# Kernel optimization log

Measured on AMD Instinct MI355X. Metric: run time of the kernel, lower is better.

The kernel has to match this reference:

```python
import jax, jax.numpy as jnp
import numpy as np

B, S, V, H, L, NH, DH, F, T = 256, 64, 21128, 768, 12, 12, 64, 3072, 11


def _layernorm(x, g, b):
    m = x.mean(-1, keepdims=True)
    v = ((x - m) ** 2).mean(-1, keepdims=True)
    return (x - m) / jnp.sqrt(v + 1e-12) * g + b


def setup_inputs():
    key = jax.random.key(0)
    ks = iter(jax.random.split(key, 24))
    std = 0.02
    w = lambda shape: jax.random.normal(next(ks), shape, jnp.float32) * std
    return {
        "input_ids": jax.random.randint(next(ks), (B, S), 0, V),
        "attention_mask": jnp.ones((B, S), jnp.int32),
        "label": jax.random.randint(next(ks), (B, S), 0, T),
        "word_emb": w((V, H)),
        "pos_emb": w((S, H)),
        "tok_emb": w((2, H)),
        "emb_ln_g": jnp.ones((H,), jnp.float32),
        "emb_ln_b": jnp.zeros((H,), jnp.float32),
        "Wqkv": w((L, H, 3 * H)),
        "bqkv": jnp.zeros((L, 3 * H), jnp.float32),
        "Wo": w((L, H, H)),
        "bo": jnp.zeros((L, H), jnp.float32),
        "ln1_g": jnp.ones((L, H), jnp.float32),
        "ln1_b": jnp.zeros((L, H), jnp.float32),
        "W1": w((L, H, F)),
        "b1": jnp.zeros((L, F), jnp.float32),
        "W2": w((L, F, H)),
        "b2": jnp.zeros((L, H), jnp.float32),
        "ln2_g": jnp.ones((L, H), jnp.float32),
        "ln2_b": jnp.zeros((L, H), jnp.float32),
        "fc_w": w((H, T)),
        "fc_b": jnp.zeros((T,), jnp.float32),
        "crf_start": w((T,)),
        "crf_end": w((T,)),
        "crf_trans": w((T, T)),
    }


def _encode(ids, mask, word_emb, pos_emb, tok_emb, eg, eb, layer_params):
    x = word_emb[ids] + pos_emb[None] + tok_emb[0][None, None]  # [B,S,H]
    x = _layernorm(x, eg, eb)
    bias = (1.0 - mask.astype(x.dtype))[:, None, None, :] * -1e9  # [B,1,1,S]

    def layer(x, p):
        Wqkv, bqkv, Wo, bo, g1, b1n, W1, b1, W2, b2, g2, b2n = p
        q, k, v = jnp.split(x @ Wqkv + bqkv, 3, axis=-1)
        sh = lambda t: t.reshape(B, S, NH, DH).transpose(0, 2, 1, 3)
        att = jax.nn.softmax(
            jnp.einsum("bhqd,bhkd->bhqk", sh(q), sh(k)) / jnp.sqrt(jnp.float32(DH)) + bias, -1
        )
        o = jnp.einsum("bhqk,bhkd->bhqd", att, sh(v)).transpose(0, 2, 1, 3).reshape(B, S, H)
        x = _layernorm(x + o @ Wo + bo, g1, b1n)
        h = jax.nn.gelu(x @ W1 + b1)
        x = _layernorm(x + h @ W2 + b2, g2, b2n)
        return x, None

    x, _ = jax.lax.scan(layer, x, layer_params)
    return x


def _crf_llh(em, tags, maskf, start, end, trans):
    # torchcrf log-likelihood, batch_first. em:[B,S,T] tags:[B,S] maskf:[B,S]
    bidx = jnp.arange(B)
    score = start[tags[:, 0]] + em[bidx, 0, tags[:, 0]]

    def num_step(s, xs):
        e_t, tp, tc, m = xs
        return s + (trans[tp, tc] + e_t[bidx, tc]) * m, None

    score, _ = jax.lax.scan(
        num_step, score,
        (em[:, 1:].transpose(1, 0, 2), tags[:, :-1].T, tags[:, 1:].T, maskf[:, 1:].T),
    )
    last_idx = maskf.sum(-1).astype(jnp.int32) - 1
    score = score + end[tags[bidx, last_idx]]

    alpha = start[None] + em[:, 0]  # [B,T]

    def den_step(a, xs):
        e_t, m = xs
        nxt = jax.scipy.special.logsumexp(a[:, :, None] + trans[None] + e_t[:, None, :], axis=1)
        return jnp.where(m[:, None] > 0, nxt, a), None

    alpha, _ = jax.lax.scan(den_step, alpha, (em[:, 1:].transpose(1, 0, 2), maskf[:, 1:].T))
    denom = jax.scipy.special.logsumexp(alpha + end[None], axis=1)
    return score - denom


def _viterbi(em, maskf, start, end, trans):
    bidx = jnp.arange(B)

    def step(s, xs):
        e_t, m = xs
        cand = s[:, :, None] + trans[None]  # [B,T_prev,T_cur]
        best_prev = jnp.argmax(cand, axis=1)  # [B,T]
        ns = jnp.max(cand, axis=1) + e_t
        return jnp.where(m[:, None] > 0, ns, s), best_prev

    score, hist = jax.lax.scan(
        step, start[None] + em[:, 0], (em[:, 1:].transpose(1, 0, 2), maskf[:, 1:].T)
    )  # hist: [S-1,B,T]
    last = jnp.argmax(score + end[None], axis=1)  # [B]

    def back(t, xs):
        h, m = xs
        nt = jnp.where(m > 0, h[bidx, t], t)
        return nt, nt

    _, prev_tags = jax.lax.scan(back, last, (hist, maskf[:, 1:].T), reverse=True)
    return jnp.concatenate([prev_tags.transpose(1, 0), last[:, None]], axis=1)  # [B,S]


def reference(input_ids, attention_mask, label, word_emb, pos_emb, tok_emb, emb_ln_g, emb_ln_b,
              Wqkv, bqkv, Wo, bo, ln1_g, ln1_b, W1, b1, W2, b2, ln2_g, ln2_b,
              fc_w, fc_b, crf_start, crf_end, crf_trans):
    lp = (Wqkv, bqkv, Wo, bo, ln1_g, ln1_b, W1, b1, W2, b2, ln2_g, ln2_b)
    x = _encode(input_ids, attention_mask, word_emb, pos_emb, tok_emb, emb_ln_g, emb_ln_b, lp)
    logits = x @ fc_w + fc_b  # [B,S,T]
    maskf = attention_mask.astype(jnp.float32)
    loss = -jnp.mean(_crf_llh(logits, label, maskf, crf_start, crf_end, crf_trans))
    pred = _viterbi(logits, maskf, crf_start, crf_end, crf_trans)
    return pred, loss
```

## Files before the change

kernel.cpp:

```cpp
#include <hip/hip_runtime.h>
#include <hip/hip_bf16.h>
#include <math.h>

namespace {

constexpr int B = 256, S = 64, H = 768, L = 12, NH = 12, F = 3072, T = 11;
constexpr int BS = B * S;
constexpr int RC = 8192;
constexpr int NCH = BS / RC;

typedef __attribute__((ext_vector_type(8))) short short8;
typedef __attribute__((ext_vector_type(4))) float f32x4;

__device__ __forceinline__ float gelu_tanh(float v) {
  float u = 0.7978845608028654f * (v + 0.044715f * v * v * v);
  u = fminf(fmaxf(u, -10.f), 10.f);
  float t = __expf(2.f * u);
  return 0.5f * v * (1.0f + (t - 1.f) / (t + 1.f));
}

__device__ __forceinline__ ushort f2bf(float v) {
  union { float f; unsigned u; } c; c.f = v;
  unsigned r = (c.u + 0x7fffu + ((c.u >> 16) & 1u)) >> 16;
  return (ushort)r;
}
__device__ __forceinline__ float bf2f(ushort u) {
  union { unsigned u; float f; } c; c.u = ((unsigned)u) << 16;
  return c.f;
}
__device__ __forceinline__ uint packhl(float v) {
  ushort hi = f2bf(v);
  ushort lo = f2bf(v - bf2f(hi));
  return (uint)hi | ((uint)lo << 16);
}
__device__ __forceinline__ float unpackhl(uint u) {
  union { unsigned u; float f; } a, b;
  a.u = u << 16;
  b.u = u & 0xffff0000u;
  return a.f + b.f;
}

__device__ __forceinline__ uint prm(uint a, uint b, uint s) {
#if __has_builtin(__builtin_amdgcn_perm)
  return __builtin_amdgcn_perm(a, b, s);
#else
  uint r = 0;
  for (int i = 0; i < 4; ++i) {
    uint sel = (s >> (8 * i)) & 0xff;
    uint byte = sel < 4 ? (b >> (8 * sel)) & 0xff : (a >> (8 * (sel - 4))) & 0xff;
    r |= byte << (8 * i);
  }
  return r;
#endif
}

union S8U { uint u[4]; short8 s; };

__device__ __forceinline__ void unpack_frag(uint4 v0, uint4 v1, short8& hi, short8& lo) {
  S8U h, l;
  h.u[0] = prm(v0.y, v0.x, 0x05040100u);
  l.u[0] = prm(v0.y, v0.x, 0x07060302u);
  h.u[1] = prm(v0.w, v0.z, 0x05040100u);
  l.u[1] = prm(v0.w, v0.z, 0x07060302u);
  h.u[2] = prm(v1.y, v1.x, 0x05040100u);
  l.u[2] = prm(v1.y, v1.x, 0x07060302u);
  h.u[3] = prm(v1.w, v1.z, 0x05040100u);
  l.u[3] = prm(v1.w, v1.z, 0x07060302u);
  hi = h.s;
  lo = l.s;
}

#define GLOAD_LDS16(gptr, ldsptr)                                                        \
  __builtin_amdgcn_global_load_lds((const __attribute__((address_space(1))) void*)(gptr), \
                                   (__attribute__((address_space(3))) void*)(ldsptr), 16, 0, 0)

template <int MODE>
__global__ __launch_bounds__(256, 2) void gemm_mfma(const uint* __restrict__ A,
                                                    const ushort* __restrict__ Bw,
                                                    const float* __restrict__ bias,
                                                    float* __restrict__ outF,
                                                    uint* __restrict__ outU,
                                                    int lda, int ldb2, int ldc,
                                                    int ldcF, int zStrideF, int ktiles) {
  __shared__ uint sA[2][128 * 32];
  __shared__ ushort sB[2][128 * 64];
  const int tid = threadIdx.x;
  const int w = tid >> 6;
  const int lane = tid & 63;
  const int wm = w >> 1;
  const int wn = w & 1;

  const int gx = gridDim.x, gy = gridDim.y;
  const int flat = ((int)blockIdx.z * gy + blockIdx.y) * gx + blockIdx.x;
  const int q8 = (gx * gy * (int)gridDim.z) >> 3;
  const int swz = (flat & 7) * q8 + (flat >> 3);
  const int bx = swz % gx;
  const int by = (swz / gx) % gy;
  const int bz = swz / (gx * gy);
  const int bm = by * 128;
  const int bn = bx * 128;
  const int kA0 = bz * ktiles * 32;
  const int kB0 = bz * ktiles * 64;

  const int srow = lane >> 3;
  const int sblk = (lane & 7) ^ srow;
  const uint* Ab = A + (size_t)(bm + w * 32 + srow) * lda + kA0 + sblk * 4;
  const ushort* Bb = Bw + (size_t)(bn + w * 32 + srow) * ldb2 + kB0 + sblk * 8;

#define STAGE(buf, tk)                                                            \
  do {                                                                            \
    _Pragma("unroll") for (int i_ = 0; i_ < 4; ++i_) {                            \
      GLOAD_LDS16(Ab + (size_t)(tk) * 32 + (size_t)(i_ * 8) * lda,                \
                  &sA[buf][(w * 32 + i_ * 8) * 32]);                              \
      GLOAD_LDS16(Bb + (size_t)(tk) * 64 + (size_t)(i_ * 8) * ldb2,               \
                  &sB[buf][(w * 32 + i_ * 8) * 64]);                              \
    }                                                                             \
  } while (0)

  const int fr = lane & 15;
  const int s7 = fr & 7;
  const int jb = lane >> 4;
  const int p0 = ((jb << 1) ^ s7) << 2;
  const int p1 = (((jb << 1) ^ s7) ^ 1) << 2;
  const int bhOff = (jb ^ s7) << 3;
  const int blOff = ((4 + jb) ^ s7) << 3;

  f32x4 acc[4][4] = {};
  const int NT = ktiles;

  STAGE(0, 0);
  asm volatile("s_waitcnt vmcnt(0)" ::: "memory");
  __builtin_amdgcn_s_barrier();

  for (int t = 0; t < NT; ++t) {
    const int cur = t & 1;
    if (t + 1 < NT) STAGE(cur ^ 1, t + 1);

    short8 ah[4], al[4];
#pragma unroll
    for (int mi = 0; mi < 4; ++mi) {
      const uint* baseA = &sA[cur][(wm * 64 + mi * 16 + fr) * 32];
      uint4 v0 = *(const uint4*)(baseA + p0);
      uint4 v1 = *(const uint4*)(baseA + p1);
      unpack_frag(v0, v1, ah[mi], al[mi]);
    }
#pragma unroll
    for (int ni = 0; ni < 4; ++ni) {
      const ushort* baseB = &sB[cur][(wn * 64 + ni * 16 + fr) * 64];
      short8 bh = *(const short8*)(baseB + bhOff);
      short8 bl = *(const short8*)(baseB + blOff);
      __builtin_amdgcn_s_setprio(1);
#pragma unroll
      for (int mi = 0; mi < 4; ++mi) {
        acc[mi][ni] = __builtin_amdgcn_mfma_f32_16x16x32_bf16(ah[mi], bh, acc[mi][ni], 0, 0, 0);
        acc[mi][ni] = __builtin_amdgcn_mfma_f32_16x16x32_bf16(ah[mi], bl, acc[mi][ni], 0, 0, 0);
        acc[mi][ni] = __builtin_amdgcn_mfma_f32_16x16x32_bf16(al[mi], bh, acc[mi][ni], 0, 0, 0);
      }
      __builtin_amdgcn_s_setprio(0);
      if (ni == 3) asm volatile("s_waitcnt vmcnt(0)" ::: "memory");
      __builtin_amdgcn_s_barrier();
    }
  }
#undef STAGE

  const int erow = jb << 2;
#pragma unroll
  for (int ni = 0; ni < 4; ++ni) {
    const int col = bn + wn * 64 + ni * 16 + fr;
    const float bv = (MODE == 3) ? 0.f : bias[col];
#pragma unroll
    for (int mi = 0; mi < 4; ++mi) {
#pragma unroll
      for (int e = 0; e < 4; ++e) {
        const int row = bm + wm * 64 + mi * 16 + erow + e;
        float v = acc[mi][ni][e] + bv;
        if (MODE == 1) {
          outU[(size_t)row * ldc + col] = packhl(gelu_tanh(v));
        } else if (MODE == 2) {
          outU[(size_t)row * ldc + col] = packhl(v);
        } else {
          outF[(size_t)bz * zStrideF + (size_t)row * ldcF + col] = v;
        }
      }
    }
  }
}

__global__ __launch_bounds__(256) void convert_w_t(const float* __restrict__ W,
                                                   ushort* __restrict__ WI, int K, int N) {
  __shared__ float tile[32][33];
  const int kb = blockIdx.y * 32, nb = blockIdx.x * 32;
  const int tr = threadIdx.x >> 5;
  const int tc = threadIdx.x & 31;
#pragma unroll
  for (int p = 0; p < 4; ++p) {
    int r = tr + p * 8;
    tile[r][tc] = W[(size_t)(kb + r) * N + nb + tc];
  }
  __syncthreads();
  const int kblk = kb >> 5;
#pragma unroll
  for (int p = 0; p < 4; ++p) {
    int n = tr + p * 8;
    float v = tile[tc][n];
    ushort hi = f2bf(v);
    ushort lo = f2bf(v - bf2f(hi));
    size_t o = (size_t)(nb + n) * (2 * K) + (size_t)kblk * 64 + tc;
    WI[o] = hi;
    WI[o + 32] = lo;
  }
}

__global__ __launch_bounds__(256) void attn_kernel(uint* __restrict__ qkv,
                                                   const int* __restrict__ mask) {
  __shared__ float smem[64 * 64 + 64 * 66 + 64 * 64];
  float (*Qs)[64] = (float (*)[64])smem;
  float (*KsT)[66] = (float (*)[66])(smem + 64 * 64);
  float (*Vs)[64] = (float (*)[64])(smem + 64 * 64 + 64 * 66);
  float (*Ps)[65] = (float (*)[65])smem;

  const int bl = blockIdx.x / NH;
  const int hh = blockIdx.x % NH;
  const int tid = threadIdx.x;
  const int lane = tid & 63;
  const int w = tid >> 6;

  for (int i = 0; i < 16; ++i) {
    int idx = tid + i * 256;
    int r = idx >> 6, d = idx & 63;
    size_t base = (size_t)(bl * 64 + r) * (3 * H) + hh * 64 + d;
    Qs[r][d] = unpackhl(qkv[base]);
    KsT[d][r] = unpackhl(qkv[base + H]);
    Vs[r][d] = unpackhl(qkv[base + 2 * H]);
  }
  __syncthreads();

  float sc[16];
#pragma unroll
  for (int i = 0; i < 16; ++i) sc[i] = 0.f;
  for (int d = 0; d < 64; ++d) {
    float kv = KsT[d][lane];
#pragma unroll
    for (int i = 0; i < 16; ++i) sc[i] += Qs[w + 4 * i][d] * kv;
  }
  __syncthreads();
  float biask = (1.0f - (float)mask[bl * S + lane]) * -1e9f;
#pragma unroll
  for (int i = 0; i < 16; ++i) Ps[w + 4 * i][lane] = sc[i] * 0.125f + biask;
  __syncthreads();

  if (tid < 64) {
    int qr = tid;
    float mx = -1e30f;
    for (int k = 0; k < 64; ++k) mx = fmaxf(mx, Ps[qr][k]);
    float sum = 0.f;
    for (int k = 0; k < 64; ++k) {
      float e = expf(Ps[qr][k] - mx);
      Ps[qr][k] = e;
      sum += e;
    }
    float inv = 1.0f / sum;
    for (int k = 0; k < 64; ++k) Ps[qr][k] *= inv;
  }
  __syncthreads();

  float o[16];
#pragma unroll
  for (int i = 0; i < 16; ++i) o[i] = 0.f;
  for (int k = 0; k < 64; ++k) {
    float vv = Vs[k][lane];
#pragma unroll
    for (int i = 0; i < 16; ++i) o[i] += Ps[w + 4 * i][k] * vv;
  }
#pragma unroll
  for (int i = 0; i < 16; ++i) {
    int qr = w + 4 * i;
    qkv[(size_t)(bl * 64 + qr) * (3 * H) + hh * 64 + lane] = packhl(o[i]);
  }
}

__global__ __launch_bounds__(256) void embed_ln_kernel(const int* __restrict__ ids,
                                                       const float* __restrict__ we,
                                                       const float* __restrict__ pe,
                                                       const float* __restrict__ te,
                                                       const float* __restrict__ g,
                                                       const float* __restrict__ bta,
                                                       uint* __restrict__ xhl) {
  __shared__ float buf[H];
  __shared__ float red[256];
  const int row = blockIdx.x;
  const int s = row % S;
  const int tid = threadIdx.x;
  const int id = ids[row];
  float local = 0.f;
  for (int i = tid; i < H; i += 256) {
    float v = we[(size_t)id * H + i] + pe[(size_t)s * H + i] + te[i];
    buf[i] = v;
    local += v;
  }
  red[tid] = local;
  __syncthreads();
  for (int st = 128; st > 0; st >>= 1) {
    if (tid < st) red[tid] += red[tid + st];
    __syncthreads();
  }
  float mean = red[0] * (1.0f / H);
  __syncthreads();
  float ls = 0.f;
  for (int i = tid; i < H; i += 256) {
    float d = buf[i] - mean;
    ls += d * d;
  }
  red[tid] = ls;
  __syncthreads();
  for (int st = 128; st > 0; st >>= 1) {
    if (tid < st) red[tid] += red[tid + st];
    __syncthreads();
  }
  float inv = 1.0f / sqrtf(red[0] * (1.0f / H) + 1e-12f);
  for (int i = tid; i < H; i += 256) {
    float o = (buf[i] - mean) * inv * g[i] + bta[i];
    xhl[(size_t)row * H + i] = packhl(o);
  }
}

__global__ __launch_bounds__(256) void add_ln_kernel(uint* __restrict__ xhl,
                                                     const float* __restrict__ pz0,
                                                     const float* __restrict__ pz1,
                                                     int prs,
                                                     const float* __restrict__ biasv,
                                                     const float* __restrict__ g,
                                                     const float* __restrict__ bta) {
  __shared__ float buf[H];
  __shared__ float red[256];
  const size_t row = blockIdx.x;
  const int tid = threadIdx.x;
  float local = 0.f;
  for (int i = tid; i < H; i += 256) {
    float v = unpackhl(xhl[row * H + i]) + ((pz0[row * (size_t)prs + i] + pz1[row * (size_t)prs + i]) + biasv[i]);
    buf[i] = v;
    local += v;
  }
  red[tid] = local;
  __syncthreads();
  for (int st = 128; st > 0; st >>= 1) {
    if (tid < st) red[tid] += red[tid + st];
    __syncthreads();
  }
  float mean = red[0] * (1.0f / H);
  __syncthreads();
  float ls = 0.f;
  for (int i = tid; i < H; i += 256) {
    float d = buf[i] - mean;
    ls += d * d;
  }
  red[tid] = ls;
  __syncthreads();
  for (int st = 128; st > 0; st >>= 1) {
    if (tid < st) red[tid] += red[tid + st];
    __syncthreads();
  }
  float inv = 1.0f / sqrtf(red[0] * (1.0f / H) + 1e-12f);
  for (int i = tid; i < H; i += 256) {
    float o = (buf[i] - mean) * inv * g[i] + bta[i];
    xhl[row * H + i] = packhl(o);
  }
}

__global__ __launch_bounds__(256) void fc_kernel(const uint* __restrict__ xhl,
                                                 const float* __restrict__ w,
                                                 const float* __restrict__ bias,
                                                 float* __restrict__ logits) {
  __shared__ float xs[H];
  const size_t row = blockIdx.x;
  const int tid = threadIdx.x;
  for (int i = tid; i < H; i += 256) xs[i] = unpackhl(xhl[row * H + i]);
  __syncthreads();
  const int j = tid >> 4, l = tid & 15;
  if (j < T) {
    float s = 0.f;
    for (int k = l; k < H; k += 16) s += xs[k] * w[(size_t)k * T + j];
#pragma unroll
    for (int d = 8; d > 0; d >>= 1) s += __shfl_down(s, d, 16);
    if (l == 0) logits[row * T + j] = s + bias[j];
  }
}

__global__ __launch_bounds__(64) void crf_llh_kernel(const float* __restrict__ em,
                                                     const int* __restrict__ label,
                                                     const int* __restrict__ mask,
                                                     const float* __restrict__ start,
                                                     const float* __restrict__ endw,
                                                     const float* __restrict__ trans,
                                                     float* __restrict__ llh) {
  const int b = blockIdx.x;
  const int c = threadIdx.x;
  __shared__ float alpha[T];
  __shared__ float tr[T][T];
  for (int i = c; i < T * T; i += 64) tr[i / T][i % T] = trans[i];
  if (c < T) alpha[c] = start[c] + em[(size_t)b * S * T + c];
  __syncthreads();
  for (int s = 1; s < S; ++s) {
    float a = 0.f;
    if (c < T) {
      float mx = -1e30f;
      for (int p = 0; p < T; ++p) mx = fmaxf(mx, alpha[p] + tr[p][c]);
      float sum = 0.f;
      for (int p = 0; p < T; ++p) sum += expf(alpha[p] + tr[p][c] - mx);
      a = mx + logf(sum) + em[((size_t)b * S + s) * T + c];
    }
    __syncthreads();
    if (c < T) {
      float m = (float)mask[b * S + s];
      alpha[c] = (m > 0.f) ? a : alpha[c];
    }
    __syncthreads();
  }
  if (c == 0) {
    float mx = -1e30f;
    for (int p = 0; p < T; ++p) mx = fmaxf(mx, alpha[p] + endw[p]);
    float sum = 0.f;
    for (int p = 0; p < T; ++p) sum += expf(alpha[p] + endw[p] - mx);
    float denom = mx + logf(sum);

    int t0 = label[b * S];
    float score = start[t0] + em[(size_t)b * S * T + t0];
    int prev = t0;
    for (int s = 1; s < S; ++s) {
      int tc = label[b * S + s];
      float m = (float)mask[b * S + s];
      score += (tr[prev][tc] + em[((size_t)b * S + s) * T + tc]) * m;
      prev = tc;
    }
    int msum = 0;
    for (int s = 0; s < S; ++s) msum += mask[b * S + s];
    score += endw[label[b * S + (msum - 1)]];
    llh[b] = score - denom;
  }
}

__global__ __launch_bounds__(256) void loss_kernel(const float* __restrict__ llh,
                                                   float* __restrict__ out) {
  __shared__ float red[256];
  const int tid = threadIdx.x;
  red[tid] = llh[tid];
  __syncthreads();
  for (int st = 128; st > 0; st >>= 1) {
    if (tid < st) red[tid] += red[tid + st];
    __syncthreads();
  }
  if (tid == 0) out[BS] = -red[0] * (1.0f / B);
}

__global__ __launch_bounds__(64) void viterbi_kernel(const float* __restrict__ em,
                                                     const int* __restrict__ mask,
                                                     const float* __restrict__ start,
                                                     const float* __restrict__ endw,
                                                     const float* __restrict__ trans,
                                                     float* __restrict__ pred) {
  const int b = blockIdx.x;
  const int c = threadIdx.x;
  __shared__ float sc[T];
  __shared__ float tr[T][T];
  __shared__ int hist[S - 1][T];
  for (int i = c; i < T * T; i += 64) tr[i / T][i % T] = trans[i];
  if (c < T) sc[c] = start[c] + em[(size_t)b * S * T + c];
  __syncthreads();
  for (int s = 1; s < S; ++s) {
    float bestv = -1e30f;
    int bestp = 0;
    if (c < T) {
      for (int p = 0; p < T; ++p) {
        float v = sc[p] + tr[p][c];
        if (v > bestv) { bestv = v; bestp = p; }
      }
      hist[s - 1][c] = bestp;
    }
    __syncthreads();
    if (c < T) {
      float m = (float)mask[b * S + s];
      sc[c] = (m > 0.f) ? (bestv + em[((size_t)b * S + s) * T + c]) : sc[c];
    }
    __syncthreads();
  }
  if (c == 0) {
    float bv = -1e30f;
    int last = 0;
    for (int p = 0; p < T; ++p) {
      float v = sc[p] + endw[p];
      if (v > bv) { bv = v; last = p; }
    }
    pred[b * S + (S - 1)] = (float)last;
    int t = last;
    for (int hs = S - 2; hs >= 0; --hs) {
      if (mask[b * S + hs + 1] > 0) t = hist[hs][t];
      pred[b * S + hs] = (float)t;
    }
  }
}

}

extern "C" void kernel_launch(void* const* d_in, const int* in_sizes, int n_in,
                              void* d_out, int out_size, void* d_ws, size_t ws_size,
                              hipStream_t stream) {
  (void)in_sizes; (void)n_in; (void)out_size; (void)ws_size;
  const int* input_ids = (const int*)d_in[0];
  const int* attn_mask = (const int*)d_in[1];
  const int* label = (const int*)d_in[2];
  const float* word_emb = (const float*)d_in[3];
  const float* pos_emb = (const float*)d_in[4];
  const float* tok_emb = (const float*)d_in[5];
  const float* eg = (const float*)d_in[6];
  const float* ebt = (const float*)d_in[7];
  const float* Wqkv = (const float*)d_in[8];
  const float* bqkv = (const float*)d_in[9];
  const float* Wo = (const float*)d_in[10];
  const float* bo = (const float*)d_in[11];
  const float* ln1g = (const float*)d_in[12];
  const float* ln1b = (const float*)d_in[13];
  const float* W1 = (const float*)d_in[14];
  const float* b1 = (const float*)d_in[15];
  const float* W2 = (const float*)d_in[16];
  const float* b2 = (const float*)d_in[17];
  const float* ln2g = (const float*)d_in[18];
  const float* ln2b = (const float*)d_in[19];
  const float* fc_w = (const float*)d_in[20];
  const float* fc_b = (const float*)d_in[21];
  const float* crf_start = (const float*)d_in[22];
  const float* crf_end = (const float*)d_in[23];
  const float* crf_trans = (const float*)d_in[24];
  float* out = (float*)d_out;

  char* p = (char*)d_ws;
  uint* xhl = (uint*)p;        p += (size_t)BS * H * 4;
  ushort* wQ = (ushort*)p;     p += (size_t)3 * H * 2 * H * 2;
  ushort* wO = (ushort*)p;     p += (size_t)H * 2 * H * 2;
  ushort* wF1 = (ushort*)p;    p += (size_t)F * 2 * H * 2;
  ushort* wF2 = (ushort*)p;    p += (size_t)H * 2 * F * 2;
  uint* big = (uint*)p;        p += (size_t)BS * 3 * H * 4;
  float* logits = (float*)p;   p += (size_t)BS * T * 4;
  float* llh = (float*)p;      p += (size_t)B * 4;
  uint* qkvU = big;
  uint* hU = big;
  float* pf = (float*)(big + (size_t)RC * F);
  float* qf = (float*)qkvU;

  embed_ln_kernel<<<BS, 256, 0, stream>>>(input_ids, word_emb, pos_emb, tok_emb, eg, ebt, xhl);

  for (int l = 0; l < L; ++l) {
    const float* wqkv_l = Wqkv + (size_t)l * H * 3 * H;
    const float* bqkv_l = bqkv + (size_t)l * 3 * H;
    const float* wo_l = Wo + (size_t)l * H * H;
    const float* bo_l = bo + (size_t)l * H;
    const float* g1 = ln1g + (size_t)l * H;
    const float* be1 = ln1b + (size_t)l * H;
    const float* w1_l = W1 + (size_t)l * H * F;
    const float* b1_l = b1 + (size_t)l * F;
    const float* w2_l = W2 + (size_t)l * F * H;
    const float* b2_l = b2 + (size_t)l * H;
    const float* g2 = ln2g + (size_t)l * H;
    const float* be2 = ln2b + (size_t)l * H;

    convert_w_t<<<dim3(3 * H / 32, H / 32), 256, 0, stream>>>(wqkv_l, wQ, H, 3 * H);
    convert_w_t<<<dim3(H / 32, H / 32), 256, 0, stream>>>(wo_l, wO, H, H);
    convert_w_t<<<dim3(F / 32, H / 32), 256, 0, stream>>>(w1_l, wF1, H, F);
    convert_w_t<<<dim3(H / 32, F / 32), 256, 0, stream>>>(w2_l, wF2, F, H);

    gemm_mfma<2><<<dim3(3 * H / 128, BS / 128, 1), 256, 0, stream>>>(
        xhl, wQ, bqkv_l, nullptr, qkvU, H, 2 * H, 3 * H, 0, 0, H / 32);
    attn_kernel<<<B * NH, 256, 0, stream>>>(qkvU, attn_mask);
    gemm_mfma<3><<<dim3(H / 128, BS / 128, 2), 256, 0, stream>>>(
        qkvU, wO, nullptr, qf + H, nullptr, 3 * H, 2 * H, 0, 3 * H, H, H / 64);
    add_ln_kernel<<<BS, 256, 0, stream>>>(xhl, qf + H, qf + 2 * H, 3 * H, bo_l, g1, be1);

    for (int ch = 0; ch < NCH; ++ch) {
      gemm_mfma<1><<<dim3(F / 128, RC / 128, 1), 256, 0, stream>>>(
          xhl + (size_t)ch * RC * H, wF1, b1_l, nullptr, hU, H, 2 * H, F, 0, 0, H / 32);
      gemm_mfma<3><<<dim3(H / 128, RC / 128, 2), 256, 0, stream>>>(
          hU, wF2, nullptr, pf, nullptr, F, 2 * F, 0, H, RC * H, F / 64);
      add_ln_kernel<<<RC, 256, 0, stream>>>(xhl + (size_t)ch * RC * H, pf, pf + (size_t)RC * H,
                                            H, b2_l, g2, be2);
    }
  }

  fc_kernel<<<BS, 256, 0, stream>>>(xhl, fc_w, fc_b, logits);
  crf_llh_kernel<<<B, 64, 0, stream>>>(logits, label, attn_mask, crf_start, crf_end, crf_trans, llh);
  loss_kernel<<<1, 256, 0, stream>>>(llh, out);
  viterbi_kernel<<<B, 64, 0, stream>>>(logits, attn_mask, crf_start, crf_end, crf_trans, out);
}
```

Before: 11.61 ms.

## Store activations in blocked hi/lo bf16 layout matching weight layout

Result: faster. 11.27 ms (-3.0%).

```diff
diff --git a/kernel.cpp b/kernel.cpp
--- a/kernel.cpp
+++ b/kernel.cpp
@@ -28,61 +28,28 @@
   union { unsigned u; float f; } c; c.u = ((unsigned)u) << 16;
   return c.f;
 }
-__device__ __forceinline__ uint packhl(float v) {
-  ushort hi = f2bf(v);
-  ushort lo = f2bf(v - bf2f(hi));
-  return (uint)hi | ((uint)lo << 16);
-}
-__device__ __forceinline__ float unpackhl(uint u) {
-  union { unsigned u; float f; } a, b;
-  a.u = u << 16;
-  b.u = u & 0xffff0000u;
-  return a.f + b.f;
-}
-
-__device__ __forceinline__ uint prm(uint a, uint b, uint s) {
-#if __has_builtin(__builtin_amdgcn_perm)
-  return __builtin_amdgcn_perm(a, b, s);
-#else
-  uint r = 0;
-  for (int i = 0; i < 4; ++i) {
-    uint sel = (s >> (8 * i)) & 0xff;
-    uint byte = sel < 4 ? (b >> (8 * sel)) & 0xff : (a >> (8 * (sel - 4))) & 0xff;
-    r |= byte << (8 * i);
-  }
-  return r;
-#endif
-}
-
-union S8U { uint u[4]; short8 s; };
-
-__device__ __forceinline__ void unpack_frag(uint4 v0, uint4 v1, short8& hi, short8& lo) {
-  S8U h, l;
-  h.u[0] = prm(v0.y, v0.x, 0x05040100u);
-  l.u[0] = prm(v0.y, v0.x, 0x07060302u);
-  h.u[1] = prm(v0.w, v0.z, 0x05040100u);
-  l.u[1] = prm(v0.w, v0.z, 0x07060302u);
-  h.u[2] = prm(v1.y, v1.x, 0x05040100u);
-  l.u[2] = prm(v1.y, v1.x, 0x07060302u);
-  h.u[3] = prm(v1.w, v1.z, 0x05040100u);
-  l.u[3] = prm(v1.w, v1.z, 0x07060302u);
-  hi = h.s;
-  lo = l.s;
-}
+__device__ __forceinline__ void split2(float v, ushort& hi, ushort& lo) {
+  hi = f2bf(v);
+  lo = f2bf(v - bf2f(hi));
+}
+__device__ __forceinline__ float join2(ushort hi, ushort lo) {
+  return bf2f(hi) + bf2f(lo);
+}
+__device__ __forceinline__ int pcol(int c) { return ((c >> 5) << 6) + (c & 31); }
 
 #define GLOAD_LDS16(gptr, ldsptr)                                                        \
   __builtin_amdgcn_global_load_lds((const __attribute__((address_space(1))) void*)(gptr), \
                                    (__attribute__((address_space(3))) void*)(ldsptr), 16, 0, 0)
 
 template <int MODE>
-__global__ __launch_bounds__(256, 2) void gemm_mfma(const uint* __restrict__ A,
+__global__ __launch_bounds__(256, 2) void gemm_mfma(const ushort* __restrict__ A,
                                                     const ushort* __restrict__ Bw,
                                                     const float* __restrict__ bias,
                                                     float* __restrict__ outF,
-                                                    uint* __restrict__ outU,
-                                                    int lda, int ldb2, int ldc,
+                                                    ushort* __restrict__ outU,
+                                                    int lda2, int ldb2, int ldc2,
                                                     int ldcF, int zStrideF, int ktiles) {
-  __shared__ uint sA[2][128 * 32];
+  __shared__ ushort sA[2][128 * 64];
   __shared__ ushort sB[2][128 * 64];
   const int tid = threadIdx.x;
   const int w = tid >> 6;
@@ -99,19 +66,18 @@
   const int bz = swz / (gx * gy);
   const int bm = by * 128;
   const int bn = bx * 128;
-  const int kA0 = bz * ktiles * 32;
-  const int kB0 = bz * ktiles * 64;
+  const int k0 = bz * ktiles * 64;
 
   const int srow = lane >> 3;
   const int sblk = (lane & 7) ^ srow;
-  const uint* Ab = A + (size_t)(bm + w * 32 + srow) * lda + kA0 + sblk * 4;
-  const ushort* Bb = Bw + (size_t)(bn + w * 32 + srow) * ldb2 + kB0 + sblk * 8;
+  const ushort* Ab = A + (size_t)(bm + w * 32 + srow) * lda2 + k0 + sblk * 8;
+  const ushort* Bb = Bw + (size_t)(bn + w * 32 + srow) * ldb2 + k0 + sblk * 8;
 
 #define STAGE(buf, tk)                                                            \
   do {                                                                            \
     _Pragma("unroll") for (int i_ = 0; i_ < 4; ++i_) {                            \
-      GLOAD_LDS16(Ab + (size_t)(tk) * 32 + (size_t)(i_ * 8) * lda,                \
-                  &sA[buf][(w * 32 + i_ * 8) * 32]);                              \
+      GLOAD_LDS16(Ab + (size_t)(tk) * 64 + (size_t)(i_ * 8) * lda2,               \
+                  &sA[buf][(w * 32 + i_ * 8) * 64]);                              \
       GLOAD_LDS16(Bb + (size_t)(tk) * 64 + (size_t)(i_ * 8) * ldb2,               \
                   &sB[buf][(w * 32 + i_ * 8) * 64]);                              \
     }                                                                             \
@@ -120,10 +86,8 @@
   const int fr = lane & 15;
   const int s7 = fr & 7;
   const int jb = lane >> 4;
-  const int p0 = ((jb << 1) ^ s7) << 2;
-  const int p1 = (((jb << 1) ^ s7) ^ 1) << 2;
-  const int bhOff = (jb ^ s7) << 3;
-  const int blOff = ((4 + jb) ^ s7) << 3;
+  const int hOff = (jb ^ s7) << 3;
+  const int lOff = ((4 + jb) ^ s7) << 3;
 
   f32x4 acc[4][4] = {};
   const int NT = ktiles;
@@ -139,16 +103,15 @@
     short8 ah[4], al[4];
 #pragma unroll
     for (int mi = 0; mi < 4; ++mi) {
-      const uint* baseA = &sA[cur][(wm * 64 + mi * 16 + fr) * 32];
-      uint4 v0 = *(const uint4*)(baseA + p0);
-      uint4 v1 = *(const uint4*)(baseA + p1);
-      unpack_frag(v0, v1, ah[mi], al[mi]);
+      const ushort* baseA = &sA[cur][(wm * 64 + mi * 16 + fr) * 64];
+      ah[mi] = *(const short8*)(baseA + hOff);
+      al[mi] = *(const short8*)(baseA + lOff);
     }
 #pragma unroll
     for (int ni = 0; ni < 4; ++ni) {
       const ushort* baseB = &sB[cur][(wn * 64 + ni * 16 + fr) * 64];
-      short8 bh = *(const short8*)(baseB + bhOff);
-      short8 bl = *(const short8*)(baseB + blOff);
+      short8 bh = *(const short8*)(baseB + hOff);
+      short8 bl = *(const short8*)(baseB + lOff);
       __builtin_amdgcn_s_setprio(1);
 #pragma unroll
       for (int mi = 0; mi < 4; ++mi) {
@@ -168,16 +131,19 @@
   for (int ni = 0; ni < 4; ++ni) {
     const int col = bn + wn * 64 + ni * 16 + fr;
     const float bv = (MODE == 3) ? 0.f : bias[col];
+    const int cb = pcol(col);
 #pragma unroll
     for (int mi = 0; mi < 4; ++mi) {
 #pragma unroll
       for (int e = 0; e < 4; ++e) {
         const int row = bm + wm * 64 + mi * 16 + erow + e;
         float v = acc[mi][ni][e] + bv;
-        if (MODE == 1) {
-          outU[(size_t)row * ldc + col] = packhl(gelu_tanh(v));
-        } else if (MODE == 2) {
-          outU[(size_t)row * ldc + col] = packhl(v);
+        if (MODE == 1 || MODE == 2) {
+          if (MODE == 1) v = gelu_tanh(v);
+          ushort hi, lo;
+          split2(v, hi, lo);
+          outU[(size_t)row * ldc2 + cb] = hi;
+          outU[(size_t)row * ldc2 + cb + 32] = lo;
         } else {
           outF[(size_t)bz * zStrideF + (size_t)row * ldcF + col] = v;
         }
@@ -203,15 +169,15 @@
   for (int p = 0; p < 4; ++p) {
     int n = tr + p * 8;
     float v = tile[tc][n];
-    ushort hi = f2bf(v);
-    ushort lo = f2bf(v - bf2f(hi));
+    ushort hi, lo;
+    split2(v, hi, lo);
     size_t o = (size_t)(nb + n) * (2 * K) + (size_t)kblk * 64 + tc;
     WI[o] = hi;
     WI[o + 32] = lo;
   }
 }
 
-__global__ __launch_bounds__(256) void attn_kernel(uint* __restrict__ qkv,
+__global__ __launch_bounds__(256) void attn_kernel(ushort* __restrict__ qkv,
                                                    const int* __restrict__ mask) {
   __shared__ float smem[64 * 64 + 64 * 66 + 64 * 64];
   float (*Qs)[64] = (float (*)[64])smem;
@@ -228,10 +194,11 @@
   for (int i = 0; i < 16; ++i) {
     int idx = tid + i * 256;
     int r = idx >> 6, d = idx & 63;
-    size_t base = (size_t)(bl * 64 + r) * (3 * H) + hh * 64 + d;
-    Qs[r][d] = unpackhl(qkv[base]);
-    KsT[d][r] = unpackhl(qkv[base + H]);
-    Vs[r][d] = unpackhl(qkv[base + 2 * H]);
+    size_t rowb = (size_t)(bl * 64 + r) * 4608;
+    int off = hh * 128 + pcol(d);
+    Qs[r][d] = join2(qkv[rowb + off], qkv[rowb + off + 32]);
+    KsT[d][r] = join2(qkv[rowb + 1536 + off], qkv[rowb + 1536 + off + 32]);
+    Vs[r][d] = join2(qkv[rowb + 3072 + off], qkv[rowb + 3072 + off + 32]);
   }
   __syncthreads();
 
@@ -272,10 +239,15 @@
 #pragma unroll
     for (int i = 0; i < 16; ++i) o[i] += Ps[w + 4 * i][k] * vv;
   }
+  const int ooff = hh * 128 + pcol(lane);
 #pragma unroll
   for (int i = 0; i < 16; ++i) {
     int qr = w + 4 * i;
-    qkv[(size_t)(bl * 64 + qr) * (3 * H) + hh * 64 + lane] = packhl(o[i]);
+    size_t rowb = (size_t)(bl * 64 + qr) * 4608;
+    ushort hi, lo;
+    split2(o[i], hi, lo);
+    qkv[rowb + ooff] = hi;
+    qkv[rowb + ooff + 32] = lo;
   }
 }
 
@@ -285,7 +257,7 @@
                                                        const float* __restrict__ te,
                                                        const float* __restrict__ g,
                                                        const float* __restrict__ bta,
-                                                       uint* __restrict__ xhl) {
+                                                       ushort* __restrict__ xhl) {
   __shared__ float buf[H];
   __shared__ float red[256];
   const int row = blockIdx.x;
@@ -320,11 +292,15 @@
   float inv = 1.0f / sqrtf(red[0] * (1.0f / H) + 1e-12f);
   for (int i = tid; i < H; i += 256) {
     float o = (buf[i] - mean) * inv * g[i] + bta[i];
-    xhl[(size_t)row * H + i] = packhl(o);
-  }
-}
-
-__global__ __launch_bounds__(256) void add_ln_kernel(uint* __restrict__ xhl,
+    int cb = pcol(i);
+    ushort hi, lo;
+    split2(o, hi, lo);
+    xhl[(size_t)row * (2 * H) + cb] = hi;
+    xhl[(size_t)row * (2 * H) + cb + 32] = lo;
+  }
+}
+
+__global__ __launch_bounds__(256) void add_ln_kernel(ushort* __restrict__ xhl,
                                                      const float* __restrict__ pz0,
                                                      const float* __restrict__ pz1,
                                                      int prs,
@@ -337,7 +313,9 @@
   const int tid = threadIdx.x;
   float local = 0.f;
   for (int i = tid; i < H; i += 256) {
-    float v = unpackhl(xhl[row * H + i]) + ((pz0[row * (size_t)prs + i] + pz1[row * (size_t)prs + i]) + biasv[i]);
+    int cb = pcol(i);
+    float v = join2(xhl[row * (2 * H) + cb], xhl[row * (2 * H) + cb + 32]) +
+              ((pz0[row * (size_t)prs + i] + pz1[row * (size_t)prs + i]) + biasv[i]);
     buf[i] = v;
     local += v;
   }
@@ -363,18 +341,25 @@
   float inv = 1.0f / sqrtf(red[0] * (1.0f / H) + 1e-12f);
   for (int i = tid; i < H; i += 256) {
     float o = (buf[i] - mean) * inv * g[i] + bta[i];
-    xhl[row * H + i] = packhl(o);
-  }
-}
-
-__global__ __launch_bounds__(256) void fc_kernel(const uint* __restrict__ xhl,
+    int cb = pcol(i);
+    ushort hi, lo;
+    split2(o, hi, lo);
+    xhl[row * (2 * H) + cb] = hi;
+    xhl[row * (2 * H) + cb + 32] = lo;
+  }
+}
+
+__global__ __launch_bounds__(256) void fc_kernel(const ushort* __restrict__ xhl,
                                                  const float* __restrict__ w,
                                                  const float* __restrict__ bias,
                                                  float* __restrict__ logits) {
   __shared__ float xs[H];
   const size_t row = blockIdx.x;
   const int tid = threadIdx.x;
-  for (int i = tid; i < H; i += 256) xs[i] = unpackhl(xhl[row * H + i]);
+  for (int i = tid; i < H; i += 256) {
+    int cb = pcol(i);
+    xs[i] = join2(xhl[row * (2 * H) + cb], xhl[row * (2 * H) + cb + 32]);
+  }
   __syncthreads();
   const int j = tid >> 4, l = tid & 15;
   if (j < T) {
@@ -533,18 +518,18 @@
   float* out = (float*)d_out;
 
   char* p = (char*)d_ws;
-  uint* xhl = (uint*)p;        p += (size_t)BS * H * 4;
+  ushort* xhl = (ushort*)p;    p += (size_t)BS * 2 * H * 2;
   ushort* wQ = (ushort*)p;     p += (size_t)3 * H * 2 * H * 2;
   ushort* wO = (ushort*)p;     p += (size_t)H * 2 * H * 2;
   ushort* wF1 = (ushort*)p;    p += (size_t)F * 2 * H * 2;
   ushort* wF2 = (ushort*)p;    p += (size_t)H * 2 * F * 2;
-  uint* big = (uint*)p;        p += (size_t)BS * 3 * H * 4;
+  char* big = p;               p += (size_t)BS * 3 * H * 4;
   float* logits = (float*)p;   p += (size_t)BS * T * 4;
   float* llh = (float*)p;      p += (size_t)B * 4;
-  uint* qkvU = big;
-  uint* hU = big;
-  float* pf = (float*)(big + (size_t)RC * F);
-  float* qf = (float*)qkvU;
+  ushort* qkvP = (ushort*)big;
+  float* qf = (float*)big;
+  ushort* hU = (ushort*)big;
+  float* pf = (float*)(big + (size_t)RC * F * 4);
 
   embed_ln_kernel<<<BS, 256, 0, stream>>>(input_ids, word_emb, pos_emb, tok_emb, eg, ebt, xhl);
 
@@ -568,19 +553,20 @@
     convert_w_t<<<dim3(H / 32, F / 32), 256, 0, stream>>>(w2_l, wF2, F, H);
 
     gemm_mfma<2><<<dim3(3 * H / 128, BS / 128, 1), 256, 0, stream>>>(
-        xhl, wQ, bqkv_l, nullptr, qkvU, H, 2 * H, 3 * H, 0, 0, H / 32);
-    attn_kernel<<<B * NH, 256, 0, stream>>>(qkvU, attn_mask);
+        xhl, wQ, bqkv_l, nullptr, qkvP, 2 * H, 2 * H, 2 * 3 * H, 0, 0, H / 32);
+    attn_kernel<<<B * NH, 256, 0, stream>>>(qkvP, attn_mask);
     gemm_mfma<3><<<dim3(H / 128, BS / 128, 2), 256, 0, stream>>>(
-        qkvU, wO, nullptr, qf + H, nullptr, 3 * H, 2 * H, 0, 3 * H, H, H / 64);
+        qkvP, wO, nullptr, qf + H, nullptr, 2 * 3 * H, 2 * H, 0, 3 * H, H, H / 64);
     add_ln_kernel<<<BS, 256, 0, stream>>>(xhl, qf + H, qf + 2 * H, 3 * H, bo_l, g1, be1);
 
     for (int ch = 0; ch < NCH; ++ch) {
       gemm_mfma<1><<<dim3(F / 128, RC / 128, 1), 256, 0, stream>>>(
-          xhl + (size_t)ch * RC * H, wF1, b1_l, nullptr, hU, H, 2 * H, F, 0, 0, H / 32);
+          xhl + (size_t)ch * RC * 2 * H, wF1, b1_l, nullptr, hU, 2 * H, 2 * H, 2 * F,
+          0, 0, H / 32);
       gemm_mfma<3><<<dim3(H / 128, RC / 128, 2), 256, 0, stream>>>(
-          hU, wF2, nullptr, pf, nullptr, F, 2 * F, 0, H, RC * H, F / 64);
-      add_ln_kernel<<<RC, 256, 0, stream>>>(xhl + (size_t)ch * RC * H, pf, pf + (size_t)RC * H,
-                                            H, b2_l, g2, be2);
+          hU, wF2, nullptr, pf, nullptr, 2 * F, 2 * F, 0, H, RC * H, F / 64);
+      add_ln_kernel<<<RC, 256, 0, stream>>>(xhl + (size_t)ch * RC * 2 * H, pf,
+                                            pf + (size_t)RC * H, H, b2_l, g2, be2);
     }
   }
 
```
